# Optimization experiments

Hardware: AMD Instinct MI355X
Metric: run time of the kernel (lower is better)

The kernel has to match this reference:

```python
import jax, jax.numpy as jnp
import numpy as np


def channel_attention(x):
    # Faithful to torch: proj_key = x.view(B, -1, C) is a memory RESHAPE, not a transpose.
    B, C, H, W = x.shape
    N = H * W
    pq = x.reshape(B, C, N)          # [B, C, N]
    pk = x.reshape(B, N, C)          # [B, N, C] -- reshape, NOT pq transposed
    attn = jax.nn.softmax(jnp.einsum('bcn,bnd->bcd', pq, pk), axis=-1)  # [B, C, C]
    out = jnp.einsum('bcd,bdn->bcn', attn, pq).reshape(B, C, H, W)
    return out + x


def positional_attention(x):
    B, C, H, W = x.shape
    N = H * W
    pk = x.reshape(B, C, N)                                  # [B, C, N]
    # proj_query = pk transposed -> attn[b, n, m] over spatial positions
    attn = jax.nn.softmax(jnp.einsum('bcn,bcm->bnm', pk, pk), axis=-1)  # [B, N, N]
    # out = bmm(pk, attn^T): out[b, c, m] = sum_n pk[b, c, n] * attn[b, m, n]
    out = jnp.einsum('bcn,bmn->bcm', pk, attn).reshape(B, C, H, W)
    return out + x


def setup_inputs() -> dict:
    key = jax.random.key(0)
    x = jax.random.normal(key, (4, 512, 64, 64), dtype=jnp.float32)
    return {"x": x}


def reference(x):
    x_ca = channel_attention(x)
    x_pa = positional_attention(x_ca)
    return x_pa
```

## Files before the change

### kernel.cpp

```cpp
#include <hip/hip_runtime.h>

#define BATCH 4
#define CH 512
#define NSP 4096

typedef __attribute__((ext_vector_type(8))) short bfrag8;
typedef __attribute__((ext_vector_type(4))) float f32x4;
typedef unsigned short u16;

#define AS1 __attribute__((address_space(1)))
#define AS3 __attribute__((address_space(3)))
__device__ __forceinline__ void gload16(const void* g, void* l) {
    __builtin_amdgcn_global_load_lds((const AS1 void*)g, (AS3 void*)l, 16, 0, 0);
}

__device__ __forceinline__ void split_bf16(float y, u16& h, u16& l) {
    unsigned int u = __float_as_uint(y);
    h = (u16)(u >> 16);
    float r = y - __uint_as_float(((unsigned int)h) << 16);
    l = (u16)(__float_as_uint(r) >> 16);
}
__device__ __forceinline__ float join_bf16(u16 h, u16 l) {
    return __uint_as_float(((unsigned int)h) << 16) + __uint_as_float(((unsigned int)l) << 16);
}

__global__ __launch_bounds__(256) void k_prep_cn(const float* __restrict__ X,
                                                 u16* __restrict__ XHi,
                                                 u16* __restrict__ XLo,
                                                 u16* __restrict__ XT1hi,
                                                 u16* __restrict__ XT1lo) {
    __shared__ unsigned int t[64][65];
    const size_t boff = (size_t)blockIdx.z * CH * NSP;
    const int c0 = blockIdx.y * 64, n0 = blockIdx.x * 64;
    const int r = threadIdx.x >> 4, col4 = (threadIdx.x & 15) * 4;
#pragma unroll
    for (int it = 0; it < 4; it++) {
        int rl = r + it * 16;
        float4 v = *(const float4*)(X + boff + (size_t)(c0 + rl) * NSP + n0 + col4);
        ushort4 h, l;
        split_bf16(v.x, h.x, l.x);
        split_bf16(v.y, h.y, l.y);
        split_bf16(v.z, h.z, l.z);
        split_bf16(v.w, h.w, l.w);
        *(ushort4*)(XHi + boff + (size_t)(c0 + rl) * NSP + n0 + col4) = h;
        *(ushort4*)(XLo + boff + (size_t)(c0 + rl) * NSP + n0 + col4) = l;
        t[rl][col4 + 0] = ((unsigned int)h.x << 16) | l.x;
        t[rl][col4 + 1] = ((unsigned int)h.y << 16) | l.y;
        t[rl][col4 + 2] = ((unsigned int)h.z << 16) | l.z;
        t[rl][col4 + 3] = ((unsigned int)h.w << 16) | l.w;
    }
    __syncthreads();
#pragma unroll
    for (int it = 0; it < 4; it++) {
        int cl = r + it * 16;
        unsigned int p0 = t[col4 + 0][cl];
        unsigned int p1 = t[col4 + 1][cl];
        unsigned int p2 = t[col4 + 2][cl];
        unsigned int p3 = t[col4 + 3][cl];
        ushort4 hv, lv;
        hv.x = p0 >> 16; hv.y = p1 >> 16; hv.z = p2 >> 16; hv.w = p3 >> 16;
        lv.x = p0 & 0xffff; lv.y = p1 & 0xffff; lv.z = p2 & 0xffff; lv.w = p3 & 0xffff;
        *(ushort4*)(XT1hi + boff + (size_t)(n0 + cl) * CH + c0 + col4) = hv;
        *(ushort4*)(XT1lo + boff + (size_t)(n0 + cl) * CH + c0 + col4) = lv;
    }
}

__global__ __launch_bounds__(256) void k_prep_nc(const float* __restrict__ X,
                                                 u16* __restrict__ XT2hi,
                                                 u16* __restrict__ XT2lo) {
    __shared__ unsigned int t[64][65];
    const size_t boff = (size_t)blockIdx.z * CH * NSP;
    const int n0 = blockIdx.x * 64, d0 = blockIdx.y * 64;
    const int r = threadIdx.x >> 4, col4 = (threadIdx.x & 15) * 4;
#pragma unroll
    for (int it = 0; it < 4; it++) {
        int rl = r + it * 16;
        float4 v = *(const float4*)(X + boff + (size_t)(n0 + rl) * CH + d0 + col4);
        ushort4 h, l;
        split_bf16(v.x, h.x, l.x);
        split_bf16(v.y, h.y, l.y);
        split_bf16(v.z, h.z, l.z);
        split_bf16(v.w, h.w, l.w);
        t[rl][col4 + 0] = ((unsigned int)h.x << 16) | l.x;
        t[rl][col4 + 1] = ((unsigned int)h.y << 16) | l.y;
        t[rl][col4 + 2] = ((unsigned int)h.z << 16) | l.z;
        t[rl][col4 + 3] = ((unsigned int)h.w << 16) | l.w;
    }
    __syncthreads();
#pragma unroll
    for (int it = 0; it < 4; it++) {
        int cl = r + it * 16;
        unsigned int p0 = t[col4 + 0][cl];
        unsigned int p1 = t[col4 + 1][cl];
        unsigned int p2 = t[col4 + 2][cl];
        unsigned int p3 = t[col4 + 3][cl];
        ushort4 hv, lv;
        hv.x = p0 >> 16; hv.y = p1 >> 16; hv.z = p2 >> 16; hv.w = p3 >> 16;
        lv.x = p0 & 0xffff; lv.y = p1 & 0xffff; lv.z = p2 & 0xffff; lv.w = p3 & 0xffff;
        *(ushort4*)(XT2hi + boff + (size_t)(d0 + cl) * NSP + n0 + col4) = hv;
        *(ushort4*)(XT2lo + boff + (size_t)(d0 + cl) * NSP + n0 + col4) = lv;
    }
}

__global__ __launch_bounds__(256, 2) void k1_mfma(const u16* __restrict__ XHi,
                                                  const u16* __restrict__ XLo,
                                                  const u16* __restrict__ XT2hi,
                                                  const u16* __restrict__ XT2lo,
                                                  float* __restrict__ Pk) {
    __shared__ __align__(16) char smem[32768];
    char* Ahi = smem;
    char* Alo = smem + 8192;
    char* Bhi = smem + 16384;
    char* Blo = smem + 24576;
    const int bid = blockIdx.x;
    const int xcd = bid & 7;
    const int i1 = bid >> 3;
    const int group = xcd * 4 + (i1 >> 4);
    const int b = group >> 3, kz = group & 7;
    const int tile = i1 & 15;
    const int c0 = (tile >> 2) * 128, d0 = (tile & 3) * 128;
    const size_t boff = (size_t)b * CH * NSP;
    const int tid = threadIdx.x, lane = tid & 63, w = tid >> 6;
    const int wr = w >> 1, wc = w & 1;
    const int rl = lane >> 2;
    const int cb = (lane & 3) * 8;
    f32x4 acc[4][4];
#pragma unroll
    for (int i = 0; i < 4; i++)
#pragma unroll
        for (int j = 0; j < 4; j++) acc[i][j] = (f32x4){0.f, 0.f, 0.f, 0.f};

    const int kbeg = kz * 512, kend = kbeg + 512;
    for (int k0 = kbeg; k0 < kend; k0 += 32) {
#pragma unroll
        for (int s = 0; s < 2; s++) {
            int idx = w * 2 + s;
            int row = 16 * idx + rl;
            gload16(XHi + boff + (size_t)(c0 + row) * NSP + k0 + cb, Ahi + idx * 1024);
            gload16(XLo + boff + (size_t)(c0 + row) * NSP + k0 + cb, Alo + idx * 1024);
            gload16(XT2hi + boff + (size_t)(d0 + row) * NSP + k0 + cb, Bhi + idx * 1024);
            gload16(XT2lo + boff + (size_t)(d0 + row) * NSP + k0 + cb, Blo + idx * 1024);
        }
        __syncthreads();
        bfrag8 ah[4], al[4], bh[4], bl[4];
        const int q16 = (lane >> 4) * 16;
        const int l15 = (lane & 15);
#pragma unroll
        for (int i = 0; i < 4; i++) {
            int offa = (wr * 64 + i * 16 + l15) * 64 + q16;
            ah[i] = *(const bfrag8*)(Ahi + offa);
            al[i] = *(const bfrag8*)(Alo + offa);
            int offb = (wc * 64 + i * 16 + l15) * 64 + q16;
            bh[i] = *(const bfrag8*)(Bhi + offb);
            bl[i] = *(const bfrag8*)(Blo + offb);
        }
#pragma unroll
        for (int i = 0; i < 4; i++)
#pragma unroll
            for (int j = 0; j < 4; j++) {
                acc[i][j] = __builtin_amdgcn_mfma_f32_16x16x32_bf16(ah[i], bh[j], acc[i][j], 0, 0, 0);
                acc[i][j] = __builtin_amdgcn_mfma_f32_16x16x32_bf16(ah[i], bl[j], acc[i][j], 0, 0, 0);
                acc[i][j] = __builtin_amdgcn_mfma_f32_16x16x32_bf16(al[i], bh[j], acc[i][j], 0, 0, 0);
            }
        __syncthreads();
    }
    float* Lb = Pk + (size_t)kz * BATCH * CH * CH + (size_t)b * CH * CH;
    const int col = lane & 15, qr = (lane >> 4) * 4;
#pragma unroll
    for (int i = 0; i < 4; i++)
#pragma unroll
        for (int j = 0; j < 4; j++)
#pragma unroll
            for (int r = 0; r < 4; r++)
                Lb[(size_t)(c0 + wr * 64 + 16 * i + qr + r) * CH + d0 + wc * 64 + 16 * j + col] =
                    acc[i][j][r];
}

__global__ __launch_bounds__(256) void k_combine8(const float* __restrict__ Pk,
                                                  float* __restrict__ Lg) {
    const size_t MM = (size_t)BATCH * CH * CH;
    size_t i = ((size_t)blockIdx.x * 256 + threadIdx.x) * 4;
    float4 s = *(const float4*)(Pk + i);
#pragma unroll
    for (int z = 1; z < 8; z++) {
        float4 v = *(const float4*)(Pk + z * MM + i);
        s.x += v.x; s.y += v.y; s.z += v.z; s.w += v.w;
    }
    *(float4*)(Lg + i) = s;
}

__global__ __launch_bounds__(256) void k_softmax_pack512(float* __restrict__ Lg) {
    __shared__ float buf[512];
    __shared__ float red[256];
    const int tid = threadIdx.x;
    float* row = Lg + (size_t)blockIdx.x * 512;
    float2 v = *(const float2*)(row + tid * 2);
    buf[tid * 2] = v.x;
    buf[tid * 2 + 1] = v.y;
    red[tid] = fmaxf(v.x, v.y);
    __syncthreads();
    for (int s = 128; s > 0; s >>= 1) {
        if (tid < s) red[tid] = fmaxf(red[tid], red[tid + s]);
        __syncthreads();
    }
    float m = red[0];
    __syncthreads();
    float e0 = __expf(buf[tid * 2] - m), e1 = __expf(buf[tid * 2 + 1] - m);
    buf[tid * 2] = e0;
    buf[tid * 2 + 1] = e1;
    red[tid] = e0 + e1;
    __syncthreads();
    for (int s = 128; s > 0; s >>= 1) {
        if (tid < s) red[tid] += red[tid + s];
        __syncthreads();
    }
    float inv = 1.0f / red[0];
    u16* u = (u16*)row;
    u16 h0, l0, h1, l1;
    split_bf16(buf[tid * 2] * inv, h0, l0);
    split_bf16(buf[tid * 2 + 1] * inv, h1, l1);
    __syncthreads();
    u[tid * 2] = h0;
    u[tid * 2 + 1] = h1;
    u[512 + tid * 2] = l0;
    u[512 + tid * 2 + 1] = l1;
}

__global__ __launch_bounds__(256, 2) void k3_mfma(const u16* __restrict__ Lu,
                                                  const u16* __restrict__ XT1hi,
                                                  const u16* __restrict__ XT1lo,
                                                  const float* __restrict__ X,
                                                  u16* __restrict__ Yhi,
                                                  u16* __restrict__ Ylo,
                                                  u16* __restrict__ YThi,
                                                  u16* __restrict__ YTlo) {
    __shared__ __align__(16) char smem[33280];
    char* Ahi = smem;
    char* Alo = smem + 8192;
    char* Bhi = smem + 16384;
    char* Blo = smem + 24576;
    const int b = blockIdx.z;
    const u16* Au = Lu + (size_t)b * CH * 1024;
    const size_t boff = (size_t)b * CH * NSP;
    const float* Xb = X + boff;
    const int tid = threadIdx.x, lane = tid & 63, w = tid >> 6;
    const int wr = w >> 1, wc = w & 1;
    const int c0 = blockIdx.y * 128, n0 = blockIdx.x * 128;
    const int rl = lane >> 2;
    const int cb = (lane & 3) * 8;
    f32x4 acc[4][4];
#pragma unroll
    for (int i = 0; i < 4; i++)
#pragma unroll
        for (int j = 0; j < 4; j++) acc[i][j] = (f32x4){0.f, 0.f, 0.f, 0.f};

    for (int k0 = 0; k0 < CH; k0 += 32) {
#pragma unroll
        for (int s = 0; s < 2; s++) {
            int idx = w * 2 + s;
            int row = 16 * idx + rl;
            gload16(Au + (size_t)(c0 + row) * 1024 + k0 + cb, Ahi + idx * 1024);
            gload16(Au + (size_t)(c0 + row) * 1024 + 512 + k0 + cb, Alo + idx * 1024);
            gload16(XT1hi + boff + (size_t)(n0 + row) * CH + k0 + cb, Bhi + idx * 1024);
            gload16(XT1lo + boff + (size_t)(n0 + row) * CH + k0 + cb, Blo + idx * 1024);
        }
        __syncthreads();
        bfrag8 ah[4], al[4], bh[4], bl[4];
        const int q16 = (lane >> 4) * 16;
        const int l15 = (lane & 15);
#pragma unroll
        for (int i = 0; i < 4; i++) {
            int offa = (wr * 64 + i * 16 + l15) * 64 + q16;
            ah[i] = *(const bfrag8*)(Ahi + offa);
            al[i] = *(const bfrag8*)(Alo + offa);
            int offb = (wc * 64 + i * 16 + l15) * 64 + q16;
            bh[i] = *(const bfrag8*)(Bhi + offb);
            bl[i] = *(const bfrag8*)(Blo + offb);
        }
#pragma unroll
        for (int i = 0; i < 4; i++)
#pragma unroll
            for (int j = 0; j < 4; j++) {
                acc[i][j] = __builtin_amdgcn_mfma_f32_16x16x32_bf16(ah[i], bh[j], acc[i][j], 0, 0, 0);
                acc[i][j] = __builtin_amdgcn_mfma_f32_16x16x32_bf16(ah[i], bl[j], acc[i][j], 0, 0, 0);
                acc[i][j] = __builtin_amdgcn_mfma_f32_16x16x32_bf16(al[i], bh[j], acc[i][j], 0, 0, 0);
            }
        __syncthreads();
    }
    u16* Yhb = Yhi + boff;
    u16* Ylb = Ylo + boff;
    u16* YThb = YThi + boff;
    u16* YTlb = YTlo + boff;
    const int col = lane & 15, qr = (lane >> 4) * 4;
    unsigned int* Tb = (unsigned int*)smem;
#pragma unroll
    for (int round = 0; round < 2; round++) {
        if (wr == round) {
            unsigned int* T = Tb + wc * 4160;
#pragma unroll
            for (int i = 0; i < 4; i++)
#pragma unroll
                for (int j = 0; j < 4; j++)
#pragma unroll
                    for (int r = 0; r < 4; r++) {
                        int cl = 16 * i + qr + r;
                        int nl = 16 * j + col;
                        int c = c0 + wr * 64 + cl;
                        int n = n0 + wc * 64 + nl;
                        float v = acc[i][j][r] + Xb[(size_t)c * NSP + n];
                        u16 h, l;
                        split_bf16(v, h, l);
                        Yhb[(size_t)c * NSP + n] = h;
                        Ylb[(size_t)c * NSP + n] = l;
                        T[nl * 65 + cl] = ((unsigned int)h << 16) | l;
                    }
        }
        __syncthreads();
        if (wr == round) {
            unsigned int* T = Tb + wc * 4160;
            const int cl = (lane & 15) * 4;
#pragma unroll
            for (int rep = 0; rep < 16; rep++) {
                int nq = rep * 4 + (lane >> 4);
                unsigned int p0 = T[nq * 65 + cl];
                unsigned int p1 = T[nq * 65 + cl + 1];
                unsigned int p2 = T[nq * 65 + cl + 2];
                unsigned int p3 = T[nq * 65 + cl + 3];
                ushort4 hv, lv;
                hv.x = p0 >> 16; hv.y = p1 >> 16; hv.z = p2 >> 16; hv.w = p3 >> 16;
                lv.x = p0 & 0xffff; lv.y = p1 & 0xffff; lv.z = p2 & 0xffff; lv.w = p3 & 0xffff;
                size_t o = (size_t)(n0 + wc * 64 + nq) * CH + c0 + wr * 64 + cl;
                *(ushort4*)(YThb + o) = hv;
                *(ushort4*)(YTlb + o) = lv;
            }
        }
        __syncthreads();
    }
}

__global__ __launch_bounds__(256, 2) void k4_mfma(const u16* __restrict__ YThi0,
                                                  const u16* __restrict__ YTlo0,
                                                  float* __restrict__ S0) {
    __shared__ __align__(16) char smem[65536];
    const int tid = threadIdx.x, lane = tid & 63, w = tid >> 6;
    const int wr = w >> 1, wc = w & 1;
    const int rb = blockIdx.y;
    const u16* Phi = YThi0 + (size_t)rb * NSP * CH;
    const u16* Plo = YTlo0 + (size_t)rb * NSP * CH;
    float* S = S0 + (size_t)rb * NSP * NSP;
    int idx = blockIdx.x;
    int bi = (int)((sqrtf(8.f * (float)idx + 1.f) - 1.f) * 0.5f);
    while ((bi + 1) * (bi + 2) / 2 <= idx) bi++;
    while (bi * (bi + 1) / 2 > idx) bi--;
    int bj = idx - bi * (bi + 1) / 2;
    const int n0 = bi * 128, m0 = bj * 128;
    const bool diag = (bi == bj);

    const int rl = lane >> 2;
    const int cb = (((lane & 3) ^ ((lane >> 3) & 3)) * 8);
    const int l15 = lane & 15;
    const int q16 = (((lane >> 4) ^ ((lane >> 1) & 3)) * 16);

    auto STAGE = [&](const u16* mat, int r0, int kt, int u) {
        char* dst = smem + (kt & 1) * 32768 + u * 8192;
        const int k0 = kt * 32;
#pragma unroll
        for (int s = 0; s < 2; s++) {
            int i2 = w * 2 + s;
            gload16(mat + (size_t)(r0 + i2 * 16 + rl) * CH + k0 + cb, dst + i2 * 1024);
        }
    };

    f32x4 acc[4][4];
#pragma unroll
    for (int i = 0; i < 4; i++)
#pragma unroll
        for (int j = 0; j < 4; j++) acc[i][j] = (f32x4){0.f, 0.f, 0.f, 0.f};
    bfrag8 ah0[4], bh0[4], ah1[4], bh1[4], al[4], bl[4];

    auto LDA = [&](const char* base, bfrag8* a) {
#pragma unroll
        for (int i = 0; i < 4; i++)
            a[i] = *(const bfrag8*)(base + (wr * 64 + i * 16 + l15) * 64 + q16);
    };
    auto LDB = [&](const char* base, bfrag8* bv) {
#pragma unroll
        for (int j = 0; j < 4; j++)
            bv[j] = *(const bfrag8*)(base + (wc * 64 + j * 16 + l15) * 64 + q16);
    };
    auto MMAp = [&](const bfrag8* a, const bfrag8* bv, auto pre) {
        __builtin_amdgcn_s_setprio(1);
        pre();
#pragma unroll
        for (int i = 0; i < 4; i++)
#pragma unroll
            for (int j = 0; j < 4; j++)
                acc[i][j] = __builtin_amdgcn_mfma_f32_16x16x32_bf16(a[i], bv[j], acc[i][j], 0, 0, 0);
        __builtin_amdgcn_s_setprio(0);
    };

#define WAITB(N)                                          \
    asm volatile("s_waitcnt vmcnt(" #N ")" ::: "memory"); \
    __builtin_amdgcn_sched_barrier(0);                    \
    __builtin_amdgcn_s_barrier();

    const char* b0 = smem;
    const char* b1 = smem + 32768;

    STAGE(Phi, n0, 0, 0);
    STAGE(Phi, m0, 0, 2);
    STAGE(Plo, n0, 0, 1);
    STAGE(Plo, m0, 0, 3);
    STAGE(Phi, n0, 1, 0);
    STAGE(Phi, m0, 1, 2);
    STAGE(Plo, n0, 1, 1);
    WAITB(10)
    LDA(b0, ah0);
    LDB(b0 + 16384, bh0);

    for (int t = 0; t < 14; t += 2) {
        STAGE(Plo, m0, t + 1, 3);
        WAITB(10)
        MMAp(ah0, bh0, [&] { LDA(b0 + 8192, al); });
        STAGE(Phi, n0, t + 2, 0);
        STAGE(Phi, m0, t + 2, 2);
        WAITB(12)
        MMAp(al, bh0, [&] { LDB(b0 + 24576, bl); });
        STAGE(Plo, n0, t + 2, 1);
        WAITB(10)
        MMAp(ah0, bl, [&] {
            LDA(b1, ah1);
            LDB(b1 + 16384, bh1);
        });
        STAGE(Plo, m0, t + 2, 3);
        WAITB(10)
        MMAp(ah1, bh1, [&] { LDA(b1 + 8192, al); });
        STAGE(Phi, n0, t + 3, 0);
        STAGE(Phi, m0, t + 3, 2);
        WAITB(12)
        MMAp(al, bh1, [&] { LDB(b1 + 24576, bl); });
        STAGE(Plo, n0, t + 3, 1);
        WAITB(10)
        MMAp(ah1, bl, [&] {
            LDA(b0, ah0);
            LDB(b0 + 16384, bh0);
        });
    }
    {
        STAGE(Plo, m0, 15, 3);
        WAITB(10)
        MMAp(ah0, bh0, [&] { LDA(b0 + 8192, al); });
        WAITB(8)
        MMAp(al, bh0, [&] { LDB(b0 + 24576, bl); });
        WAITB(4)
        MMAp(ah0, bl, [&] {
            LDA(b1, ah1);
            LDB(b1 + 16384, bh1);
        });
    }
    {
        WAITB(2)
        MMAp(ah1, bh1, [&] { LDA(b1 + 8192, al); });
        WAITB(0)
        MMAp(al, bh1, [&] { LDB(b1 + 24576, bl); });
        __builtin_amdgcn_sched_barrier(0);
        __builtin_amdgcn_s_barrier();
        MMAp(ah1, bl, [&] {});
    }
#undef WAITB

    const int col = lane & 15, qr = (lane >> 4) * 4;
#pragma unroll
    for (int i = 0; i < 4; i++)
#pragma unroll
        for (int j = 0; j < 4; j++)
#pragma unroll
            for (int r = 0; r < 4; r++)
                S[(size_t)(n0 + wr * 64 + 16 * i + qr + r) * NSP + m0 + wc * 64 + 16 * j + col] =
                    acc[i][j][r];
    if (!diag) {
        float* Tbase = (float*)smem;
#pragma unroll
        for (int round = 0; round < 2; round++) {
            __syncthreads();
            if (wr == round) {
                float* T = Tbase + wc * (64 * 68);
#pragma unroll
                for (int i = 0; i < 4; i++)
#pragma unroll
                    for (int j = 0; j < 4; j++)
#pragma unroll
                        for (int r = 0; r < 4; r++)
                            T[(16 * j + col) * 68 + 16 * i + qr + r] = acc[i][j][r];
            }
            __syncthreads();
            if (wr == round) {
                float* T = Tbase + wc * (64 * 68);
                const int rq = (lane & 15) * 4;
#pragma unroll
                for (int rep = 0; rep < 16; rep++) {
                    int cq = rep * 4 + (lane >> 4);
                    float4 v = *(const float4*)(T + cq * 68 + rq);
                    *(float4*)(S + (size_t)(m0 + wc * 64 + cq) * NSP + n0 + wr * 64 + rq) = v;
                }
            }
        }
    }
}

__global__ __launch_bounds__(256) void k_softmax_pack(float* __restrict__ S) {
    __shared__ float buf[4096];
    __shared__ float red[256];
    const int tid = threadIdx.x;
    float* row = S + (size_t)blockIdx.x * NSP;
    float m = -INFINITY;
#pragma unroll
    for (int it = 0; it < 4; it++) {
        int i = (tid + it * 256) * 4;
        float4 v = *(const float4*)(row + i);
        buf[i] = v.x; buf[i + 1] = v.y; buf[i + 2] = v.z; buf[i + 3] = v.w;
        m = fmaxf(m, fmaxf(fmaxf(v.x, v.y), fmaxf(v.z, v.w)));
    }
    red[tid] = m;
    __syncthreads();
    for (int s = 128; s > 0; s >>= 1) {
        if (tid < s) red[tid] = fmaxf(red[tid], red[tid + s]);
        __syncthreads();
    }
    m = red[0];
    __syncthreads();
    float sum = 0.f;
#pragma unroll
    for (int it = 0; it < 4; it++) {
        int i = (tid + it * 256) * 4;
        float e0 = __expf(buf[i] - m), e1 = __expf(buf[i + 1] - m);
        float e2 = __expf(buf[i + 2] - m), e3 = __expf(buf[i + 3] - m);
        buf[i] = e0; buf[i + 1] = e1; buf[i + 2] = e2; buf[i + 3] = e3;
        sum += e0 + e1 + e2 + e3;
    }
    red[tid] = sum;
    __syncthreads();
    for (int s = 128; s > 0; s >>= 1) {
        if (tid < s) red[tid] += red[tid + s];
        __syncthreads();
    }
    float inv = 1.0f / red[0];
    u16* u = (u16*)row;
#pragma unroll
    for (int it = 0; it < 4; it++) {
        int i = (tid + it * 256) * 4;
        ushort4 hv;
        hv.x = (u16)(__float_as_uint(buf[i] * inv) >> 16);
        hv.y = (u16)(__float_as_uint(buf[i + 1] * inv) >> 16);
        hv.z = (u16)(__float_as_uint(buf[i + 2] * inv) >> 16);
        hv.w = (u16)(__float_as_uint(buf[i + 3] * inv) >> 16);
        *(ushort4*)(u + i) = hv;
    }
}

__global__ __launch_bounds__(512, 2) void k6_mfma(const u16* __restrict__ Yhi0,
                                                  const u16* __restrict__ Ylo0,
                                                  const u16* __restrict__ Su,
                                                  float* __restrict__ Out0,
                                                  float* __restrict__ Pp0,
                                                  float* __restrict__ Pp1) {
    __shared__ __align__(16) char smem[73728];
    const int tid = threadIdx.x, lane = tid & 63, w = tid >> 6;
    const int wr = w >> 2, wc = w & 3;
    const int m0 = blockIdx.x * 256, c0 = blockIdx.y * 128;
    const int rb = blockIdx.z >> 1, kz = blockIdx.z & 1;
    const u16* Yhi = Yhi0 + (size_t)rb * CH * NSP;
    const u16* Ylo = Ylo0 + (size_t)rb * CH * NSP;
    const u16* Pu = Su + (size_t)rb * NSP * NSP * 2;
    float* Out = Out0 + (size_t)rb * CH * NSP;
    float* Ppart = rb ? Pp1 : Pp0;
    const int kb = kz * 2048;
    const int rl = lane >> 2;
    const int cb = (((lane & 3) ^ ((lane >> 3) & 3)) * 8);
    const int l15 = lane & 15;
    const int q16 = (((lane >> 4) ^ ((lane >> 1) & 3)) * 16);

    auto STAGE = [&](int kt, int slot) {
        char* dst = smem + slot * 24576;
        const int k0 = kb + kt * 32;
        gload16(Yhi + (size_t)(c0 + w * 16 + rl) * NSP + k0 + cb, dst + w * 1024);
#pragma unroll
        for (int s = 0; s < 2; s++) {
            int idx = w * 2 + s;
            gload16(Pu + (size_t)(m0 + idx * 16 + rl) * 8192 + k0 + cb,
                    dst + 8192 + idx * 1024);
        }
    };

    f32x4 acc[4][4];
#pragma unroll
    for (int i = 0; i < 4; i++)
#pragma unroll
        for (int j = 0; j < 4; j++) acc[i][j] = (f32x4){0.f, 0.f, 0.f, 0.f};
    bfrag8 ah[4], bh[4];

#define K6PHASE(SLOT, STSLOT, T, DOSTAGE, WN)                                            \
    {                                                                                    \
        const char* bA = smem + (SLOT)*24576;                                            \
        const char* bB = bA + 8192;                                                      \
        _Pragma("unroll") for (int i = 0; i < 4; i++) ah[i] =                            \
            *(const bfrag8*)(bA + (wr * 64 + i * 16 + l15) * 64 + q16);                  \
        _Pragma("unroll") for (int j = 0; j < 4; j++) bh[j] =                            \
            *(const bfrag8*)(bB + (wc * 64 + j * 16 + l15) * 64 + q16);                  \
        if (DOSTAGE) STAGE((T) + 2, (STSLOT));                                           \
        asm volatile("s_waitcnt vmcnt(" #WN ")" ::: "memory");                           \
        __builtin_amdgcn_sched_barrier(0);                                               \
        __builtin_amdgcn_s_barrier();                                                    \
        __builtin_amdgcn_s_setprio(1);                                                   \
        _Pragma("unroll") for (int i = 0; i < 4; i++)                                    \
            _Pragma("unroll") for (int j = 0; j < 4; j++) acc[i][j] =                    \
                __builtin_amdgcn_mfma_f32_16x16x32_bf16(ah[i], bh[j], acc[i][j], 0, 0, 0); \
        __builtin_amdgcn_s_setprio(0);                                                   \
    }

    STAGE(0, 0);
    STAGE(1, 1);
    asm volatile("s_waitcnt vmcnt(3)" ::: "memory");
    __builtin_amdgcn_sched_barrier(0);
    __builtin_amdgcn_s_barrier();

    for (int tt = 0; tt < 60; tt += 3) {
        K6PHASE(0, 2, tt, true, 3)
        K6PHASE(1, 0, tt + 1, true, 3)
        K6PHASE(2, 1, tt + 2, true, 3)
    }
    K6PHASE(0, 2, 60, true, 3)
    K6PHASE(1, 0, 61, true, 3)
    K6PHASE(2, 0, 62, false, 0)
    K6PHASE(0, 0, 63, false, 0)
#undef K6PHASE

    const int col = lane & 15, qr = (lane >> 4) * 4;
    if (kz == 0) {
#pragma unroll
        for (int i = 0; i < 4; i++)
#pragma unroll
            for (int j = 0; j < 4; j++)
#pragma unroll
                for (int r = 0; r < 4; r++) {
                    int c = c0 + wr * 64 + 16 * i + qr + r;
                    int mm = m0 + wc * 64 + 16 * j + col;
                    Out[(size_t)c * NSP + mm] =
                        acc[i][j][r] +
                        join_bf16(Yhi[(size_t)c * NSP + mm], Ylo[(size_t)c * NSP + mm]);
                }
    } else {
#pragma unroll
        for (int i = 0; i < 4; i++)
#pragma unroll
            for (int j = 0; j < 4; j++)
#pragma unroll
                for (int r = 0; r < 4; r++) {
                    int c = c0 + wr * 64 + 16 * i + qr + r;
                    int mm = m0 + wc * 64 + 16 * j + col;
                    Ppart[(size_t)c * NSP + mm] = acc[i][j][r];
                }
    }
}

__global__ __launch_bounds__(256) void k_fixup(float* __restrict__ Out0,
                                               const float* __restrict__ Pp0,
                                               const float* __restrict__ Pp1) {
    const size_t CN = (size_t)CH * NSP;
    const int b = blockIdx.y;
    const float* P = b ? Pp1 : Pp0;
    float* O = Out0 + (size_t)b * CN;
    size_t i = ((size_t)blockIdx.x * 256 + threadIdx.x) * 4;
    float4 o = *(const float4*)(O + i);
    float4 a = *(const float4*)(P + i);
    o.x += a.x; o.y += a.y; o.z += a.z; o.w += a.w;
    *(float4*)(O + i) = o;
}

extern "C" void kernel_launch(void* const* d_in, const int* in_sizes, int n_in,
                              void* d_out, int out_size, void* d_ws, size_t ws_size,
                              hipStream_t stream) {
    const float* x = (const float*)d_in[0];
    float* out = (float*)d_out;

    char* p = (char*)d_ws;
    const size_t SZ16 = (size_t)BATCH * CH * NSP * 2;
    const size_t HALF = SZ16 / 2;
    u16* XHi = (u16*)p;
    u16* XLo = (u16*)(p + SZ16);
    u16* XT2hi = (u16*)(p + 2 * SZ16);
    u16* XT2lo = (u16*)(p + 3 * SZ16);
    u16* XT1hi = (u16*)(p + 4 * SZ16);
    u16* XT1lo = (u16*)(p + 5 * SZ16);
    float* S = (float*)p;
    u16* Yhi = (u16*)(p + 8 * SZ16);
    u16* Ylo = (u16*)(p + 9 * SZ16);
    u16* YThi = (u16*)(p + 10 * SZ16);
    u16* YTlo = (u16*)(p + 11 * SZ16);
    float* Pk = (float*)(p + 8 * SZ16);
    float* Lg = (float*)(p + 12 * SZ16);

    k_prep_cn<<<dim3(NSP / 64, CH / 64, BATCH), 256, 0, stream>>>(x, XHi, XLo, XT1hi, XT1lo);
    k_prep_nc<<<dim3(NSP / 64, CH / 64, BATCH), 256, 0, stream>>>(x, XT2hi, XT2lo);
    k1_mfma<<<dim3(512), 256, 0, stream>>>(XHi, XLo, XT2hi, XT2lo, Pk);
    k_combine8<<<dim3((BATCH * CH * CH) / (4 * 256)), 256, 0, stream>>>(Pk, Lg);
    k_softmax_pack512<<<dim3(BATCH * CH), 256, 0, stream>>>(Lg);
    k3_mfma<<<dim3(NSP / 128, CH / 128, BATCH), 256, 0, stream>>>((const u16*)Lg, XT1hi, XT1lo, x,
                                                                  Yhi, Ylo, YThi, YTlo);

    const int TRI = (NSP / 128) * (NSP / 128 + 1) / 2;
    for (int round = 0; round < 2; round++) {
        const size_t b0 = (size_t)(2 * round);
        float* Pp0 = (float*)((char*)YThi + round * HALF);
        float* Pp1 = (float*)((char*)YTlo + round * HALF);
        k4_mfma<<<dim3(TRI, 2), 256, 0, stream>>>(YThi + b0 * NSP * CH, YTlo + b0 * NSP * CH, S);
        k_softmax_pack<<<dim3(2 * NSP), 256, 0, stream>>>(S);
        k6_mfma<<<dim3(NSP / 256, CH / 128, 4), 512, 0, stream>>>(Yhi + b0 * CH * NSP,
                                                                  Ylo + b0 * CH * NSP,
                                                                  (const u16*)S,
                                                                  out + b0 * CH * NSP, Pp0, Pp1);
        k_fixup<<<dim3((CH * NSP) / (4 * 256), 2), 256, 0, stream>>>(out + b0 * CH * NSP, Pp0, Pp1);
    }
}
```

Baseline: 464.9 us.

## Software-pipeline k1 channel-gram GEMM with double-buffered swizzled LDS and XCD remap in k4

Rewrites the k1 split-bf16 MFMA loop as a double-buffered pipeline. Global-to-LDS loads for the next k-tiles are issued between MFMA groups, with fine-grained vmcnt waits and raised wave priority around the MFMAs. LDS addressing gets an XOR swizzle to reduce bank conflicts. k4 remaps block indices so consecutive triangle tiles land on the same XCD for better L2 locality. The cost is double the LDS per block (64 KB), which may limit occupancy, plus hand-tuned waitcnt values that must exactly match the load order.

Result: no change. 462.8 us (-0.5%).

```diff
diff --git a/kernel.cpp b/kernel.cpp
--- a/kernel.cpp
+++ b/kernel.cpp
@@ -107,11 +107,7 @@
                                                   const u16* __restrict__ XT2hi,
                                                   const u16* __restrict__ XT2lo,
                                                   float* __restrict__ Pk) {
-    __shared__ __align__(16) char smem[32768];
-    char* Ahi = smem;
-    char* Alo = smem + 8192;
-    char* Bhi = smem + 16384;
-    char* Blo = smem + 24576;
+    __shared__ __align__(16) char smem[65536];
     const int bid = blockIdx.x;
     const int xcd = bid & 7;
     const int i1 = bid >> 3;
@@ -123,47 +119,109 @@
     const int tid = threadIdx.x, lane = tid & 63, w = tid >> 6;
     const int wr = w >> 1, wc = w & 1;
     const int rl = lane >> 2;
-    const int cb = (lane & 3) * 8;
+    const int cb = (((lane & 3) ^ ((lane >> 3) & 3)) * 8);
+    const int l15 = lane & 15;
+    const int q16 = (((lane >> 4) ^ ((lane >> 1) & 3)) * 16);
+    const int kbeg = kz * 512;
+
+    auto STAGE = [&](const u16* mat, int r0, int kt, int u) {
+        char* dst = smem + (kt & 1) * 32768 + u * 8192;
+        const int k0 = kbeg + kt * 32;
+#pragma unroll
+        for (int s = 0; s < 2; s++) {
+            int i2 = w * 2 + s;
+            gload16(mat + boff + (size_t)(r0 + i2 * 16 + rl) * NSP + k0 + cb, dst + i2 * 1024);
+        }
+    };
+
     f32x4 acc[4][4];
 #pragma unroll
     for (int i = 0; i < 4; i++)
 #pragma unroll
         for (int j = 0; j < 4; j++) acc[i][j] = (f32x4){0.f, 0.f, 0.f, 0.f};
-
-    const int kbeg = kz * 512, kend = kbeg + 512;
-    for (int k0 = kbeg; k0 < kend; k0 += 32) {
-#pragma unroll
-        for (int s = 0; s < 2; s++) {
-            int idx = w * 2 + s;
-            int row = 16 * idx + rl;
-            gload16(XHi + boff + (size_t)(c0 + row) * NSP + k0 + cb, Ahi + idx * 1024);
-            gload16(XLo + boff + (size_t)(c0 + row) * NSP + k0 + cb, Alo + idx * 1024);
-            gload16(XT2hi + boff + (size_t)(d0 + row) * NSP + k0 + cb, Bhi + idx * 1024);
-            gload16(XT2lo + boff + (size_t)(d0 + row) * NSP + k0 + cb, Blo + idx * 1024);
-        }
-        __syncthreads();
-        bfrag8 ah[4], al[4], bh[4], bl[4];
-        const int q16 = (lane >> 4) * 16;
-        const int l15 = (lane & 15);
-#pragma unroll
-        for (int i = 0; i < 4; i++) {
-            int offa = (wr * 64 + i * 16 + l15) * 64 + q16;
-            ah[i] = *(const bfrag8*)(Ahi + offa);
-            al[i] = *(const bfrag8*)(Alo + offa);
-            int offb = (wc * 64 + i * 16 + l15) * 64 + q16;
-            bh[i] = *(const bfrag8*)(Bhi + offb);
-            bl[i] = *(const bfrag8*)(Blo + offb);
-        }
+    bfrag8 ah[4], al[4], bh[4], bl[4];
+
+    auto LDA = [&](const char* base, bfrag8* a) {
 #pragma unroll
         for (int i = 0; i < 4; i++)
-#pragma unroll
-            for (int j = 0; j < 4; j++) {
-                acc[i][j] = __builtin_amdgcn_mfma_f32_16x16x32_bf16(ah[i], bh[j], acc[i][j], 0, 0, 0);
-                acc[i][j] = __builtin_amdgcn_mfma_f32_16x16x32_bf16(ah[i], bl[j], acc[i][j], 0, 0, 0);
-                acc[i][j] = __builtin_amdgcn_mfma_f32_16x16x32_bf16(al[i], bh[j], acc[i][j], 0, 0, 0);
-            }
-        __syncthreads();
-    }
+            a[i] = *(const bfrag8*)(base + (wr * 64 + i * 16 + l15) * 64 + q16);
+    };
+    auto LDB = [&](const char* base, bfrag8* bv) {
+#pragma unroll
+        for (int j = 0; j < 4; j++)
+            bv[j] = *(const bfrag8*)(base + (wc * 64 + j * 16 + l15) * 64 + q16);
+    };
+    auto MMA = [&](const bfrag8* a, const bfrag8* bv) {
+        __builtin_amdgcn_s_setprio(1);
+#pragma unroll
+        for (int i = 0; i < 4; i++)
+#pragma unroll
+            for (int j = 0; j < 4; j++)
+                acc[i][j] = __builtin_amdgcn_mfma_f32_16x16x32_bf16(a[i], bv[j], acc[i][j], 0, 0, 0);
+        __builtin_amdgcn_s_setprio(0);
+    };
+
+#define WAITB(N)                                          \
+    asm volatile("s_waitcnt vmcnt(" #N ")" ::: "memory"); \
+    __builtin_amdgcn_sched_barrier(0);                    \
+    __builtin_amdgcn_s_barrier();
+
+    STAGE(XHi, c0, 0, 0);
+    STAGE(XT2hi, d0, 0, 2);
+    STAGE(XLo, c0, 0, 1);
+    STAGE(XT2lo, d0, 0, 3);
+    STAGE(XHi, c0, 1, 0);
+    STAGE(XT2hi, d0, 1, 2);
+    STAGE(XLo, c0, 1, 1);
+    WAITB(10)
+
+    for (int t = 0; t < 14; ++t) {
+        const char* buf = smem + (t & 1) * 32768;
+        LDA(buf, ah);
+        LDB(buf + 16384, bh);
+        STAGE(XT2lo, d0, t + 1, 3);
+        WAITB(10)
+        MMA(ah, bh);
+        LDA(buf + 8192, al);
+        STAGE(XHi, c0, t + 2, 0);
+        STAGE(XT2hi, d0, t + 2, 2);
+        WAITB(12)
+        MMA(al, bh);
+        LDB(buf + 24576, bl);
+        STAGE(XLo, c0, t + 2, 1);
+        WAITB(10)
+        MMA(ah, bl);
+    }
+    {
+        const char* buf = smem;
+        LDA(buf, ah);
+        LDB(buf + 16384, bh);
+        STAGE(XT2lo, d0, 15, 3);
+        WAITB(10)
+        MMA(ah, bh);
+        LDA(buf + 8192, al);
+        WAITB(8)
+        MMA(al, bh);
+        LDB(buf + 24576, bl);
+        WAITB(4)
+        MMA(ah, bl);
+    }
+    {
+        const char* buf = smem + 32768;
+        LDA(buf, ah);
+        LDB(buf + 16384, bh);
+        WAITB(2)
+        MMA(ah, bh);
+        LDA(buf + 8192, al);
+        WAITB(0)
+        MMA(al, bh);
+        LDB(buf + 24576, bl);
+        __builtin_amdgcn_sched_barrier(0);
+        __builtin_amdgcn_s_barrier();
+        MMA(ah, bl);
+    }
+#undef WAITB
+
     float* Lb = Pk + (size_t)kz * BATCH * CH * CH + (size_t)b * CH * CH;
     const int col = lane & 15, qr = (lane >> 4) * 4;
 #pragma unroll
@@ -348,7 +406,8 @@
     const u16* Phi = YThi0 + (size_t)rb * NSP * CH;
     const u16* Plo = YTlo0 + (size_t)rb * NSP * CH;
     float* S = S0 + (size_t)rb * NSP * NSP;
-    int idx = blockIdx.x;
+    const int bid0 = blockIdx.x;
+    int idx = (bid0 & 7) * 66 + (bid0 >> 3);
     int bi = (int)((sqrtf(8.f * (float)idx + 1.f) - 1.f) * 0.5f);
     while ((bi + 1) * (bi + 2) / 2 <= idx) bi++;
     while (bi * (bi + 1) / 2 > idx) bi--;
```
